# Performance work log

Hardware: AMD Instinct MI355X
Metric: run time of the kernel (lower is better)

## Reference

```python
import jax, jax.numpy as jnp
import numpy as np

N, D, E, B, NMAX, C = 50000, 64, 800000, 50, 1000, 100


def setup_inputs() -> dict:
    key = jax.random.key(0)
    ks = jax.random.split(key, 12)
    s = 0.05
    return {
        "x": jax.random.normal(ks[0], (N, D), jnp.float32),
        "e": jax.random.normal(ks[1], (E, D), jnp.float32),
        "edge_index": jax.random.randint(ks[2], (2, E), 0, N),
        "attr1": jax.random.normal(ks[3], (B, C, D), jnp.float32),
        "nc1": jax.random.uniform(ks[4], (B, NMAX, C), jnp.float32),
        "x_idx": jnp.arange(N),
        "eps1": jnp.zeros((1,), jnp.float32),
        "eps2": jnp.zeros((1,), jnp.float32),
        "W_ma": jax.random.normal(ks[5], (2 * D, D), jnp.float32) * s,
        "b_ma": jnp.zeros((D,), jnp.float32),
        "W_mu": jax.random.normal(ks[6], (D, D), jnp.float32) * s,
        "b_mu": jnp.zeros((D,), jnp.float32),
        "W_ua": jax.random.normal(ks[7], (D, D), jnp.float32) * s,
        "b_ua": jnp.zeros((D,), jnp.float32),
        "W_uu": jax.random.normal(ks[8], (D, D), jnp.float32) * s,
        "b_uu": jnp.zeros((D,), jnp.float32),
        "W_c": jax.random.normal(ks[9], (2 * D, D), jnp.float32) * s,
        "b_c": jnp.zeros((D,), jnp.float32),
    }


def reference(x, e, edge_index, attr1, nc1, x_idx, eps1, eps2,
              W_ma, b_ma, W_mu, b_mu, W_ua, b_ua, W_uu, b_uu, W_c, b_c):
    # adjacency branch: gather -> MLP -> scatter-sum (GIN-style)
    x_j = x[edge_index[0]]                                   # [E, D]
    msg_adj = jax.nn.relu(jnp.concatenate([x_j, e], axis=-1) @ W_ma + b_ma)
    agg_adj = jax.ops.segment_sum(msg_adj, edge_index[1], num_segments=x.shape[0])
    # hierarchical pooling branch: cluster MLP then dense matmul back to nodes
    msg_up = jax.nn.relu(attr1 @ W_mu + b_mu)                # [B, C, D]
    agg_up = jnp.einsum('bnc,bcd->bnd', nc1, msg_up)         # [B, NMAX, D]
    agg_up = agg_up.reshape(-1, agg_up.shape[-1])[x_idx]     # [N, D]
    out_adj = jax.nn.relu((agg_adj + (1.0 + eps1) * x) @ W_ua + b_ua)
    out_up = jax.nn.relu((agg_up + (1.0 + eps2) * x) @ W_uu + b_uu)
    return jnp.concatenate([out_adj, out_up], axis=-1) @ W_c + b_c
```

## Files before the change

### kernel.cpp

```cpp
#include <hip/hip_runtime.h>

#define NN 50000
#define DD 64
#define EE 800000
#define BB 50
#define NMAXX 1000
#define CC 100

typedef short short8 __attribute__((ext_vector_type(8)));
typedef float float4v __attribute__((ext_vector_type(4)));

__device__ __forceinline__ float rl(float v, int l) {
  return __int_as_float(__builtin_amdgcn_readlane(__float_as_int(v), l));
}
__device__ __forceinline__ short f2bf(float f) {
  unsigned u = __float_as_uint(f);
  unsigned r = (u + 0x7fffu + ((u >> 16) & 1u)) >> 16;
  return (short)r;
}
__device__ __forceinline__ unsigned pack2(float a, float b) {
  return (unsigned)(unsigned short)f2bf(a) |
         ((unsigned)(unsigned short)f2bf(b) << 16);
}
__device__ __forceinline__ short8 pack8(const float* p) {
  union { unsigned u[4]; short8 s; } r;
  float4 v0 = *(const float4*)p;
  float4 v1 = *(const float4*)(p + 4);
  r.u[0] = pack2(v0.x, v0.y); r.u[1] = pack2(v0.z, v0.w);
  r.u[2] = pack2(v1.x, v1.y); r.u[3] = pack2(v1.z, v1.w);
  return r.s;
}


__global__ __launch_bounds__(256) void k_prep(
    const int* __restrict__ ei, const float* __restrict__ x,
    const float* __restrict__ Wma, const float* __restrict__ Wua,
    const float* __restrict__ Wuu, const float* __restrict__ Wc,
    int* __restrict__ cnt, short* __restrict__ xb,
    short* __restrict__ WtF, short* __restrict__ WtF1,
    short* __restrict__ WtF2, short* __restrict__ WtF3) {
  const int i = blockIdx.x * 256 + threadIdx.x;
  atomicAdd(&cnt[ei[EE + i]], 1);
  {
    float4 xv = *(const float4*)&x[(size_t)i * 4];
    ((uint2*)xb)[i] = make_uint2(pack2(xv.x, xv.y), pack2(xv.z, xv.w));
  }
  if (i < 8192) {
    int j = i & 7, lane = (i >> 3) & 63, cbks = i >> 9;
    int cb = cbks & 3, ks = cbks >> 2;
    int k = ks * 32 + (lane >> 4) * 8 + j;
    int n = cb * 16 + (lane & 15);
    WtF[i]  = f2bf(Wma[k * 64 + n]);
    WtF3[i] = f2bf(Wc[k * 64 + n]);
    if (i < 4096) {
      WtF1[i] = f2bf(Wua[k * 64 + n]);
      WtF2[i] = f2bf(Wuu[k * 64 + n]);
    }
  }
}

#define CHUNK 196
__global__ __launch_bounds__(256) void k_scan1(const int* __restrict__ cnt,
                                               int* __restrict__ part) {
  __shared__ int s[256];
  const int t = threadIdx.x, b = blockIdx.x;
  const int gi = b * CHUNK + t;
  s[t] = (t < CHUNK && gi < NN) ? cnt[gi] : 0;
  __syncthreads();
#pragma unroll
  for (int off = 128; off; off >>= 1) {
    if (t < off) s[t] += s[t + off];
    __syncthreads();
  }
  if (t == 0) part[b] = s[0];
}
__global__ __launch_bounds__(256) void k_scan2(const int* __restrict__ part,
                                               int* __restrict__ partx) {
  __shared__ int s[256];
  const int t = threadIdx.x;
  int v = part[t];
  s[t] = v;
  __syncthreads();
#pragma unroll
  for (int off = 1; off < 256; off <<= 1) {
    int tv = (t >= off) ? s[t - off] : 0;
    __syncthreads();
    s[t] += tv;
    __syncthreads();
  }
  partx[t] = s[t] - v;
}
__global__ __launch_bounds__(256) void k_scan3(const int* __restrict__ cnt,
                                               const int* __restrict__ partx,
                                               int* __restrict__ head) {
  __shared__ int s[256];
  const int t = threadIdx.x, b = blockIdx.x;
  const int gi = b * CHUNK + t;
  int v = (t < CHUNK && gi < NN) ? cnt[gi] : 0;
  s[t] = v;
  __syncthreads();
#pragma unroll
  for (int off = 1; off < 256; off <<= 1) {
    int tv = (t >= off) ? s[t - off] : 0;
    __syncthreads();
    s[t] += tv;
    __syncthreads();
  }
  if (t < CHUNK && gi < NN) head[gi] = partx[b] + s[t] - v;
}

__global__ __launch_bounds__(256) void k_scatter(
    const int* __restrict__ ei, int* __restrict__ head,
    uint2* __restrict__ sde) {
  const int q = blockIdx.x * 256 + threadIdx.x;
  int d = ei[EE + q];
  int pos = atomicAdd(&head[d], 1);
  sde[pos] = make_uint2((unsigned)ei[q] | ((unsigned)d << 16), (unsigned)q);
}

__global__ __launch_bounds__(256) void k_msgup(
    const float* __restrict__ attr1, const float* __restrict__ Wmu,
    const float* __restrict__ bmu, short* __restrict__ msgupT) {
  __shared__ float Wl[64 * 64];
  const int tid = threadIdx.x;
  for (int i = tid; i < 64 * 64; i += 256) Wl[i] = Wmu[i];
  __syncthreads();
  const int lane = tid & 63;
  const int row = blockIdx.x * 4 + (tid >> 6);
  float a = attr1[(size_t)row * 64 + lane];
  float acc = bmu[lane];
#pragma unroll 8
  for (int k = 0; k < 64; ++k)
    acc = fmaf(rl(a, k), Wl[k * 64 + lane], acc);
  const int b = row / 100, c = row - b * 100;
  msgupT[(size_t)b * 6400 + lane * 100 + c] = f2bf(fmaxf(acc, 0.f));
}

__global__ __launch_bounds__(256) void k_aggup(
    const float* __restrict__ nc1, const short* __restrict__ msgupT,
    float* __restrict__ aggup) {
  constexpr int LDA = 136;
  __shared__ float Ncf[64 * CC];
  __shared__ short A[64 * LDA];
  __shared__ short Wt[64 * LDA];
  const int b = blockIdx.x >> 4;
  const int tile = blockIdx.x & 15;
  const int i0 = tile * 64;
  const int tid = threadIdx.x;
  const float* ncb = nc1 + ((size_t)b * NMAXX + i0) * CC;
  for (int idx = tid; idx < 64 * CC; idx += 256) {
    int r = idx / CC;
    Ncf[idx] = (i0 + r < NMAXX) ? ncb[idx] : 0.f;
  }
  {
    const unsigned* src = (const unsigned*)(msgupT + (size_t)b * 6400);
    unsigned* dstw = (unsigned*)Wt;
    for (int i = tid; i < 64 * 50; i += 256) {
      int row = i / 50, cu = i - row * 50;
      dstw[row * 68 + cu] = src[i];
    }
    for (int i = tid; i < 64 * 14; i += 256) {
      int row = i / 14, cu = 50 + (i - row * 14);
      dstw[row * 68 + cu] = 0;
    }
  }
  __syncthreads();
  {
    const int row = tid >> 2, kp = tid & 3;
#pragma unroll
    for (int j = 0; j < 16; ++j) {
      int k = kp * 32 + 2 * j;
      unsigned u = 0;
      if (k < CC) {
        float2 v = *(const float2*)&Ncf[row * CC + k];
        u = pack2(v.x, v.y);
      }
      *(unsigned*)&A[row * LDA + k] = u;
    }
  }
  __syncthreads();
  const int lane = tid & 63;
  const int w = tid >> 6;
  const int m = lane & 15;
  const int koff = (lane >> 4) * 8;
  float4v acc[4];
#pragma unroll
  for (int cb = 0; cb < 4; ++cb) acc[cb] = (float4v)0.f;
#pragma unroll
  for (int ks = 0; ks < 4; ++ks) {
    short8 af = *(const short8*)&A[(w * 16 + m) * LDA + ks * 32 + koff];
#pragma unroll
    for (int cb = 0; cb < 4; ++cb) {
      short8 bf = *(const short8*)&Wt[(cb * 16 + m) * LDA + ks * 32 + koff];
      acc[cb] = __builtin_amdgcn_mfma_f32_16x16x32_bf16(af, bf, acc[cb], 0, 0, 0);
    }
  }
  const int rbase = (lane >> 4) * 4;
#pragma unroll
  for (int cb = 0; cb < 4; ++cb)
#pragma unroll
    for (int r = 0; r < 4; ++r) {
      int i = i0 + w * 16 + rbase + r;
      if (i < NMAXX)
        aggup[((size_t)b * NMAXX + i) * 64 + cb * 16 + m] = acc[cb][r];
    }
}

__global__ __launch_bounds__(256) void k_edge_mfma(
    const short* __restrict__ xb, const float* __restrict__ e,
    const uint2* __restrict__ sde, const short* __restrict__ WtF,
    const float* __restrict__ bma, float* __restrict__ agg) {
  __shared__ short WtL[8192];
  __shared__ float Cs[4][16][68];
  const int tid = threadIdx.x;
  const int nwg = gridDim.x;
  const int qq = nwg >> 3, rr = nwg & 7;
  const int xx = blockIdx.x & 7, oo = blockIdx.x >> 3;
  const int bid = (xx < rr ? xx * (qq + 1) : rr * (qq + 1) + (xx - rr) * qq) + oo;
  {
    const uint4* s = (const uint4*)WtF;
    uint4* d = (uint4*)WtL;
#pragma unroll
    for (int it = 0; it < 4; ++it) d[it * 256 + tid] = s[it * 256 + tid];
  }
  __syncthreads();
  const int lane = tid & 63;
  const int wv = tid >> 6;
  const int m = lane & 15;
  const int koff = (lane >> 4) * 8;
  float bias[4];
#pragma unroll
  for (int cb = 0; cb < 4; ++cb) bias[cb] = bma[cb * 16 + m];
  const int base = bid * 256 + wv * 64;
  int dprev = -1;
  float run = 0.f;
#pragma unroll
  for (int c4 = 0; c4 < 4; ++c4) {
    const int tb = base + c4 * 16;
    const uint2 v = sde[tb + m];
    const int src = (int)(v.x & 0xffffu);
    const int dst = (int)(v.x >> 16);
    const int eid = (int)v.y;
    short8 a0 = *(const short8*)(xb + (size_t)src * 64 + koff);
    short8 a1 = *(const short8*)(xb + (size_t)src * 64 + 32 + koff);
    const float* er = e + (size_t)eid * 64;
    short8 a2 = pack8(er + koff);
    short8 a3 = pack8(er + 32 + koff);
    float4v acc[4];
#pragma unroll
    for (int cb = 0; cb < 4; ++cb) acc[cb] = (float4v)0.f;
#pragma unroll
    for (int cb = 0; cb < 4; ++cb) {
      short8 b0 = *(const short8*)&WtL[((0 * 4 + cb) * 64 + lane) * 8];
      short8 b1 = *(const short8*)&WtL[((1 * 4 + cb) * 64 + lane) * 8];
      short8 b2 = *(const short8*)&WtL[((2 * 4 + cb) * 64 + lane) * 8];
      short8 b3 = *(const short8*)&WtL[((3 * 4 + cb) * 64 + lane) * 8];
      acc[cb] = __builtin_amdgcn_mfma_f32_16x16x32_bf16(a0, b0, acc[cb], 0, 0, 0);
      acc[cb] = __builtin_amdgcn_mfma_f32_16x16x32_bf16(a1, b1, acc[cb], 0, 0, 0);
      acc[cb] = __builtin_amdgcn_mfma_f32_16x16x32_bf16(a2, b2, acc[cb], 0, 0, 0);
      acc[cb] = __builtin_amdgcn_mfma_f32_16x16x32_bf16(a3, b3, acc[cb], 0, 0, 0);
    }
    const int rbase = (lane >> 4) * 4;
#pragma unroll
    for (int cb = 0; cb < 4; ++cb)
#pragma unroll
      for (int r = 0; r < 4; ++r)
        Cs[wv][rbase + r][cb * 16 + m] = fmaxf(acc[cb][r] + bias[cb], 0.f);
#pragma unroll
    for (int r = 0; r < 16; ++r) {
      int dr = __builtin_amdgcn_readlane(dst, r);
      float val = Cs[wv][r][lane];
      if (dr != dprev) {
        if (run != 0.f) atomicAdd(&agg[(size_t)dprev * 64 + lane], run);
        run = 0.f;
        dprev = dr;
      }
      run += val;
    }
  }
  if (run != 0.f) atomicAdd(&agg[(size_t)dprev * 64 + lane], run);
}

__global__ __launch_bounds__(256) void k_final(
    const float* __restrict__ x, const float* __restrict__ agg,
    const float* __restrict__ aggup, const int* __restrict__ xidx,
    const float* __restrict__ eps1, const float* __restrict__ eps2,
    const short* __restrict__ WtF1, const float* __restrict__ bua,
    const short* __restrict__ WtF2, const float* __restrict__ buu,
    const short* __restrict__ WtF3, const float* __restrict__ bc,
    float* __restrict__ out) {
  constexpr int LD1 = 72;
  constexpr int LD3 = 136;
  __shared__ short A1[64 * LD1];
  __shared__ short A2[64 * LD1];
  __shared__ short O[64 * LD3];
  const int tid = threadIdx.x;
  const float s1 = 1.f + eps1[0], s2 = 1.f + eps2[0];
  const int r0 = blockIdx.x * 64;
  {
    const int row = tid >> 2, kp = tid & 3;
    int g = r0 + row;
    if (g >= NN) g = NN - 1;
    const size_t xb_ = (size_t)g * 64 + kp * 16;
    const size_t ub = (size_t)xidx[g] * 64 + kp * 16;
#pragma unroll
    for (int j = 0; j < 4; ++j) {
      float4 xv = *(const float4*)&x[xb_ + j * 4];
      float4 av = *(const float4*)&agg[xb_ + j * 4];
      float4 uv = *(const float4*)&aggup[ub + j * 4];
      unsigned h1lo = pack2(av.x + s1 * xv.x, av.y + s1 * xv.y);
      unsigned h1hi = pack2(av.z + s1 * xv.z, av.w + s1 * xv.w);
      unsigned h2lo = pack2(uv.x + s2 * xv.x, uv.y + s2 * xv.y);
      unsigned h2hi = pack2(uv.z + s2 * xv.z, uv.w + s2 * xv.w);
      *(uint2*)&A1[row * LD1 + kp * 16 + j * 4] = make_uint2(h1lo, h1hi);
      *(uint2*)&A2[row * LD1 + kp * 16 + j * 4] = make_uint2(h2lo, h2hi);
    }
  }
  __syncthreads();
  const int lane = tid & 63;
  const int w = tid >> 6;
  const int m = lane & 15;
  const int koff = (lane >> 4) * 8;
  const int rbase = (lane >> 4) * 4;
  float4v acc1[4], acc2[4];
#pragma unroll
  for (int cb = 0; cb < 4; ++cb) { acc1[cb] = (float4v)0.f; acc2[cb] = (float4v)0.f; }
#pragma unroll
  for (int ks = 0; ks < 2; ++ks) {
    short8 a1 = *(const short8*)&A1[(w * 16 + m) * LD1 + ks * 32 + koff];
    short8 a2 = *(const short8*)&A2[(w * 16 + m) * LD1 + ks * 32 + koff];
#pragma unroll
    for (int cb = 0; cb < 4; ++cb) {
      short8 b1 = *(const short8*)&WtF1[((ks * 4 + cb) * 64 + lane) * 8];
      short8 b2 = *(const short8*)&WtF2[((ks * 4 + cb) * 64 + lane) * 8];
      acc1[cb] = __builtin_amdgcn_mfma_f32_16x16x32_bf16(a1, b1, acc1[cb], 0, 0, 0);
      acc2[cb] = __builtin_amdgcn_mfma_f32_16x16x32_bf16(a2, b2, acc2[cb], 0, 0, 0);
    }
  }
#pragma unroll
  for (int cb = 0; cb < 4; ++cb) {
    float bb1 = bua[cb * 16 + m];
    float bb2 = buu[cb * 16 + m];
#pragma unroll
    for (int r = 0; r < 4; ++r) {
      int rowL = w * 16 + rbase + r;
      O[rowL * LD3 + cb * 16 + m] = f2bf(fmaxf(acc1[cb][r] + bb1, 0.f));
      O[rowL * LD3 + 64 + cb * 16 + m] = f2bf(fmaxf(acc2[cb][r] + bb2, 0.f));
    }
  }
  __syncthreads();
  float4v acc3[4];
#pragma unroll
  for (int cb = 0; cb < 4; ++cb) acc3[cb] = (float4v)0.f;
#pragma unroll
  for (int ks = 0; ks < 4; ++ks) {
    short8 af = *(const short8*)&O[(w * 16 + m) * LD3 + ks * 32 + koff];
#pragma unroll
    for (int cb = 0; cb < 4; ++cb) {
      short8 bf = *(const short8*)&WtF3[((ks * 4 + cb) * 64 + lane) * 8];
      acc3[cb] = __builtin_amdgcn_mfma_f32_16x16x32_bf16(af, bf, acc3[cb], 0, 0, 0);
    }
  }
#pragma unroll
  for (int cb = 0; cb < 4; ++cb) {
    float bb = bc[cb * 16 + m];
#pragma unroll
    for (int r = 0; r < 4; ++r) {
      int g = r0 + w * 16 + rbase + r;
      if (g < NN)
        out[(size_t)g * 64 + cb * 16 + m] = acc3[cb][r] + bb;
    }
  }
}

extern "C" void kernel_launch(void* const* d_in, const int* in_sizes, int n_in,
                              void* d_out, int out_size, void* d_ws, size_t ws_size,
                              hipStream_t stream) {
  const float* x     = (const float*)d_in[0];
  const float* e     = (const float*)d_in[1];
  const int*   ei    = (const int*)d_in[2];
  const float* attr1 = (const float*)d_in[3];
  const float* nc1   = (const float*)d_in[4];
  const int*   xidx  = (const int*)d_in[5];
  const float* eps1  = (const float*)d_in[6];
  const float* eps2  = (const float*)d_in[7];
  const float* Wma   = (const float*)d_in[8];
  const float* bma   = (const float*)d_in[9];
  const float* Wmu   = (const float*)d_in[10];
  const float* bmu   = (const float*)d_in[11];
  const float* Wua   = (const float*)d_in[12];
  const float* bua   = (const float*)d_in[13];
  const float* Wuu   = (const float*)d_in[14];
  const float* buu   = (const float*)d_in[15];
  const float* Wc    = (const float*)d_in[16];
  const float* bc    = (const float*)d_in[17];
  float* out = (float*)d_out;

  float* agg    = (float*)d_ws;
  int*   cnt    = (int*)(agg + (size_t)NN * 64);
  float* aggup  = (float*)(cnt + NN);
  short* msgupT = (short*)(aggup + (size_t)NN * 64);
  short* xbuf   = msgupT + (size_t)BB * 6400;
  int*   head   = (int*)(xbuf + (size_t)NN * 64);
  int*   part   = head + NN;
  int*   partx  = part + 256;
  uint2* sde    = (uint2*)(partx + 256);
  short* WtF    = (short*)(sde + EE);
  short* WtF1   = WtF + 8192;
  short* WtF2   = WtF1 + 4096;
  short* WtF3   = WtF2 + 4096;

  hipMemsetAsync(agg, 0, (size_t)NN * 64 * sizeof(float) + NN * sizeof(int),
                 stream);
  k_prep<<<dim3(EE / 256), dim3(256), 0, stream>>>(
      ei, x, Wma, Wua, Wuu, Wc, cnt, xbuf, WtF, WtF1, WtF2, WtF3);
  k_scan1<<<dim3(256), dim3(256), 0, stream>>>(cnt, part);
  k_scan2<<<dim3(1), dim3(256), 0, stream>>>(part, partx);
  k_scan3<<<dim3(256), dim3(256), 0, stream>>>(cnt, partx, head);
  k_scatter<<<dim3(EE / 256), dim3(256), 0, stream>>>(ei, head, sde);
  k_msgup<<<dim3(BB * CC / 4), dim3(256), 0, stream>>>(attr1, Wmu, bmu, msgupT);
  k_aggup<<<dim3(BB * 16), dim3(256), 0, stream>>>(nc1, msgupT, aggup);
  k_edge_mfma<<<dim3(EE / 256), dim3(256), 0, stream>>>(
      xbuf, e, sde, WtF, bma, agg);
  k_final<<<dim3((NN + 63) / 64), dim3(256), 0, stream>>>(
      x, agg, aggup, xidx, eps1, eps2, WtF1, bua, WtF2, buu, WtF3, bc, out);
}
```

Before: 500.4 us.

## Replace per-node counting sort with two-level bucket sort and fuse msgup into prep

Result: faster. 463.6 us (-7.3%).

```diff
diff --git a/kernel.cpp b/kernel.cpp
--- a/kernel.cpp
+++ b/kernel.cpp
@@ -6,6 +6,9 @@
 #define BB 50
 #define NMAXX 1000
 #define CC 100
+
+#define NBKT 391
+#define BCAP 3072
 
 typedef short short8 __attribute__((ext_vector_type(8)));
 typedef float float4v __attribute__((ext_vector_type(4)));
@@ -34,106 +37,95 @@
 
 __global__ __launch_bounds__(256) void k_prep(
     const int* __restrict__ ei, const float* __restrict__ x,
-    const float* __restrict__ Wma, const float* __restrict__ Wua,
+    const float* __restrict__ attr1,
+    const float* __restrict__ Wma, const float* __restrict__ Wmu,
+    const float* __restrict__ bmu, const float* __restrict__ Wua,
     const float* __restrict__ Wuu, const float* __restrict__ Wc,
-    int* __restrict__ cnt, short* __restrict__ xb,
+    int* __restrict__ bcnt, short* __restrict__ xb,
+    uint2* __restrict__ sdeB, short* __restrict__ msgupT,
     short* __restrict__ WtF, short* __restrict__ WtF1,
     short* __restrict__ WtF2, short* __restrict__ WtF3) {
-  const int i = blockIdx.x * 256 + threadIdx.x;
-  atomicAdd(&cnt[ei[EE + i]], 1);
-  {
-    float4 xv = *(const float4*)&x[(size_t)i * 4];
-    ((uint2*)xb)[i] = make_uint2(pack2(xv.x, xv.y), pack2(xv.z, xv.w));
-  }
-  if (i < 8192) {
-    int j = i & 7, lane = (i >> 3) & 63, cbks = i >> 9;
-    int cb = cbks & 3, ks = cbks >> 2;
-    int k = ks * 32 + (lane >> 4) * 8 + j;
-    int n = cb * 16 + (lane & 15);
-    WtF[i]  = f2bf(Wma[k * 64 + n]);
-    WtF3[i] = f2bf(Wc[k * 64 + n]);
-    if (i < 4096) {
-      WtF1[i] = f2bf(Wua[k * 64 + n]);
-      WtF2[i] = f2bf(Wuu[k * 64 + n]);
-    }
-  }
-}
-
-#define CHUNK 196
-__global__ __launch_bounds__(256) void k_scan1(const int* __restrict__ cnt,
-                                               int* __restrict__ part) {
-  __shared__ int s[256];
-  const int t = threadIdx.x, b = blockIdx.x;
-  const int gi = b * CHUNK + t;
-  s[t] = (t < CHUNK && gi < NN) ? cnt[gi] : 0;
+  const int tid = threadIdx.x;
+  if (blockIdx.x < EE / 256) {
+    const int i = blockIdx.x * 256 + tid;
+    const int s = ei[i];
+    const int d = ei[EE + i];
+    const int bkt = d >> 7;
+    int pos = atomicAdd(&bcnt[bkt * 16], 1);
+    if (pos < BCAP)
+      sdeB[(size_t)bkt * BCAP + pos] =
+          make_uint2((unsigned)s | ((unsigned)d << 16), (unsigned)i);
+    {
+      float4 xv = *(const float4*)&x[(size_t)i * 4];
+      ((uint2*)xb)[i] = make_uint2(pack2(xv.x, xv.y), pack2(xv.z, xv.w));
+    }
+    if (i < 8192) {
+      int j = i & 7, lane = (i >> 3) & 63, cbks = i >> 9;
+      int cb = cbks & 3, ks = cbks >> 2;
+      int k = ks * 32 + (lane >> 4) * 8 + j;
+      int n = cb * 16 + (lane & 15);
+      WtF[i]  = f2bf(Wma[k * 64 + n]);
+      WtF3[i] = f2bf(Wc[k * 64 + n]);
+      if (i < 4096) {
+        WtF1[i] = f2bf(Wua[k * 64 + n]);
+        WtF2[i] = f2bf(Wuu[k * 64 + n]);
+      }
+    }
+  } else {
+    __shared__ float Wl[64 * 64];
+    for (int i = tid; i < 64 * 64; i += 256) Wl[i] = Wmu[i];
+    __syncthreads();
+    const int lane = tid & 63;
+    const int row = (blockIdx.x - EE / 256) * 4 + (tid >> 6);
+    float a = attr1[(size_t)row * 64 + lane];
+    float acc = bmu[lane];
+#pragma unroll 8
+    for (int k = 0; k < 64; ++k)
+      acc = fmaf(rl(a, k), Wl[k * 64 + lane], acc);
+    const int b = row / 100, c = row - b * 100;
+    msgupT[(size_t)b * 6400 + lane * 100 + c] = f2bf(fmaxf(acc, 0.f));
+  }
+}
+
+__global__ __launch_bounds__(256) void k_sort(
+    const uint2* __restrict__ sdeB, const int* __restrict__ bcnt,
+    uint2* __restrict__ sde) {
+  __shared__ uint2 Eb[BCAP];
+  __shared__ int lcnt[128];
+  __shared__ int lpos[128];
+  __shared__ int red[256];
+  const int b = blockIdx.x, t = threadIdx.x;
+  int acc = 0;
+  for (int j = t; j < b; j += 256) acc += bcnt[j * 16];
+  red[t] = acc;
   __syncthreads();
 #pragma unroll
   for (int off = 128; off; off >>= 1) {
-    if (t < off) s[t] += s[t + off];
+    if (t < off) red[t] += red[t + off];
     __syncthreads();
   }
-  if (t == 0) part[b] = s[0];
-}
-__global__ __launch_bounds__(256) void k_scan2(const int* __restrict__ part,
-                                               int* __restrict__ partx) {
-  __shared__ int s[256];
-  const int t = threadIdx.x;
-  int v = part[t];
-  s[t] = v;
-  __syncthreads();
-#pragma unroll
-  for (int off = 1; off < 256; off <<= 1) {
-    int tv = (t >= off) ? s[t - off] : 0;
-    __syncthreads();
-    s[t] += tv;
-    __syncthreads();
-  }
-  partx[t] = s[t] - v;
-}
-__global__ __launch_bounds__(256) void k_scan3(const int* __restrict__ cnt,
-                                               const int* __restrict__ partx,
-                                               int* __restrict__ head) {
-  __shared__ int s[256];
-  const int t = threadIdx.x, b = blockIdx.x;
-  const int gi = b * CHUNK + t;
-  int v = (t < CHUNK && gi < NN) ? cnt[gi] : 0;
-  s[t] = v;
-  __syncthreads();
-#pragma unroll
-  for (int off = 1; off < 256; off <<= 1) {
-    int tv = (t >= off) ? s[t - off] : 0;
-    __syncthreads();
-    s[t] += tv;
-    __syncthreads();
-  }
-  if (t < CHUNK && gi < NN) head[gi] = partx[b] + s[t] - v;
-}
-
-__global__ __launch_bounds__(256) void k_scatter(
-    const int* __restrict__ ei, int* __restrict__ head,
-    uint2* __restrict__ sde) {
-  const int q = blockIdx.x * 256 + threadIdx.x;
-  int d = ei[EE + q];
-  int pos = atomicAdd(&head[d], 1);
-  sde[pos] = make_uint2((unsigned)ei[q] | ((unsigned)d << 16), (unsigned)q);
-}
-
-__global__ __launch_bounds__(256) void k_msgup(
-    const float* __restrict__ attr1, const float* __restrict__ Wmu,
-    const float* __restrict__ bmu, short* __restrict__ msgupT) {
-  __shared__ float Wl[64 * 64];
-  const int tid = threadIdx.x;
-  for (int i = tid; i < 64 * 64; i += 256) Wl[i] = Wmu[i];
-  __syncthreads();
-  const int lane = tid & 63;
-  const int row = blockIdx.x * 4 + (tid >> 6);
-  float a = attr1[(size_t)row * 64 + lane];
-  float acc = bmu[lane];
-#pragma unroll 8
-  for (int k = 0; k < 64; ++k)
-    acc = fmaf(rl(a, k), Wl[k * 64 + lane], acc);
-  const int b = row / 100, c = row - b * 100;
-  msgupT[(size_t)b * 6400 + lane * 100 + c] = f2bf(fmaxf(acc, 0.f));
+  const int base = red[0];
+  int n = bcnt[b * 16];
+  if (n > BCAP) n = BCAP;
+  if (t < 128) lcnt[t] = 0;
+  __syncthreads();
+  for (int i = t; i < n; i += 256) {
+    uint2 v = sdeB[(size_t)b * BCAP + i];
+    Eb[i] = v;
+    atomicAdd(&lcnt[(v.x >> 16) & 127], 1);
+  }
+  __syncthreads();
+  if (t < 128) {
+    int ssum = 0;
+    for (int j = 0; j < t; ++j) ssum += lcnt[j];
+    lpos[t] = ssum;
+  }
+  __syncthreads();
+  for (int i = t; i < n; i += 256) {
+    uint2 v = Eb[i];
+    int p = atomicAdd(&lpos[(v.x >> 16) & 127], 1);
+    sde[base + p] = v;
+  }
 }
 
 __global__ __launch_bounds__(256) void k_aggup(
@@ -397,28 +389,24 @@
   float* out = (float*)d_out;
 
   float* agg    = (float*)d_ws;
-  int*   cnt    = (int*)(agg + (size_t)NN * 64);
-  float* aggup  = (float*)(cnt + NN);
+  int*   bcnt   = (int*)(agg + (size_t)NN * 64);
+  float* aggup  = (float*)(bcnt + NBKT * 16);
   short* msgupT = (short*)(aggup + (size_t)NN * 64);
   short* xbuf   = msgupT + (size_t)BB * 6400;
-  int*   head   = (int*)(xbuf + (size_t)NN * 64);
-  int*   part   = head + NN;
-  int*   partx  = part + 256;
-  uint2* sde    = (uint2*)(partx + 256);
+  uint2* sdeB   = (uint2*)(xbuf + (size_t)NN * 64);
+  uint2* sde    = sdeB + (size_t)NBKT * BCAP;
   short* WtF    = (short*)(sde + EE);
   short* WtF1   = WtF + 8192;
   short* WtF2   = WtF1 + 4096;
   short* WtF3   = WtF2 + 4096;
 
-  hipMemsetAsync(agg, 0, (size_t)NN * 64 * sizeof(float) + NN * sizeof(int),
+  hipMemsetAsync(agg, 0,
+                 (size_t)NN * 64 * sizeof(float) + NBKT * 16 * sizeof(int),
                  stream);
-  k_prep<<<dim3(EE / 256), dim3(256), 0, stream>>>(
-      ei, x, Wma, Wua, Wuu, Wc, cnt, xbuf, WtF, WtF1, WtF2, WtF3);
-  k_scan1<<<dim3(256), dim3(256), 0, stream>>>(cnt, part);
-  k_scan2<<<dim3(1), dim3(256), 0, stream>>>(part, partx);
-  k_scan3<<<dim3(256), dim3(256), 0, stream>>>(cnt, partx, head);
-  k_scatter<<<dim3(EE / 256), dim3(256), 0, stream>>>(ei, head, sde);
-  k_msgup<<<dim3(BB * CC / 4), dim3(256), 0, stream>>>(attr1, Wmu, bmu, msgupT);
+  k_prep<<<dim3(EE / 256 + BB * CC / 4), dim3(256), 0, stream>>>(
+      ei, x, attr1, Wma, Wmu, bmu, Wua, Wuu, Wc,
+      bcnt, xbuf, sdeB, msgupT, WtF, WtF1, WtF2, WtF3);
+  k_sort<<<dim3(NBKT), dim3(256), 0, stream>>>(sdeB, bcnt, sde);
   k_aggup<<<dim3(BB * 16), dim3(256), 0, stream>>>(nc1, msgupT, aggup);
   k_edge_mfma<<<dim3(EE / 256), dim3(256), 0, stream>>>(
       xbuf, e, sde, WtF, bma, agg);
```
